# Performance work log

Hardware: AMD Instinct MI355X
Metric: run time of the kernel (lower is better)

The kernel has to match this reference:

```python
import jax, jax.numpy as jnp
import numpy as np

B, T, C, A, P = 16, 1024, 512, 4096, 256  # batch, frames, phones, allophone arcs, phonemes


def setup_inputs() -> dict:
    key = jax.random.key(0)
    k1, k2, k3 = jax.random.split(key, 3)
    hs_pad = jax.random.normal(k1, (B, T, C), dtype=jnp.float32)
    # each phone has exactly A // C allophone arcs (full coverage, balanced)
    phone_arc_labels = jnp.arange(A, dtype=jnp.int32) % C
    arcs_per_phone = A // C
    # weights near -log(arcs_per_phone) so sum_a exp(log_prob + w) ~= 1,
    # matching a trained allophone layer and keeping the redis step log-safe
    alloW = 0.01 * jax.random.normal(k2, (A,), dtype=jnp.float32) - jnp.log(
        jnp.float32(arcs_per_phone)
    )
    phoneme_arc_labels = jax.random.randint(k3, (A,), 0, P, dtype=jnp.int32)
    return {
        "hs_pad": hs_pad,
        "alloW": alloW,
        "phone_arc_labels": phone_arc_labels,
        "phoneme_arc_labels": phoneme_arc_labels,
        "n_phonemes": P,
    }


def reference(hs_pad, alloW, phone_arc_labels, phoneme_arc_labels, n_phonemes):
    # log_softmax over phones
    log_probs = jax.nn.log_softmax(hs_pad, axis=-1)  # [B,T,C]
    # WFST intersection of linear emission graph with 1-state allophone graph:
    # arc a gets weight log_probs[..., phone_label(a)] + alloW[a]
    new_emissions = log_probs[..., phone_arc_labels] + alloW  # [B,T,A]
    # squash many phones per phoneme: exp + scatter-add over output labels
    ex = jnp.exp(new_emissions)
    Bq, Tq = ex.shape[0], ex.shape[1]
    squashed = jnp.zeros((Bq, Tq, n_phonemes), dtype=ex.dtype)
    squashed = squashed.at[..., phoneme_arc_labels].add(ex)  # [B,T,P]
    # redistribute probability mass so it sums to 1
    redistributed = (squashed.sum(axis=-1) - 1.0)[..., None] / n_phonemes
    squashed = squashed - redistributed
    return jnp.log(squashed)
```

## Files before the change

kernel.cpp:

```cpp
#include <hip/hip_runtime.h>
#include <hip/hip_bf16.h>

#define BT   16384
#define CDIM 512
#define ADIM 4096
#define PDIM 256

typedef __attribute__((ext_vector_type(8))) short  short8;
typedef __attribute__((ext_vector_type(8))) unsigned short ushort8;
typedef __attribute__((ext_vector_type(4))) float  f32x4;

__device__ __forceinline__ unsigned short bf16_rne(float f) {
    unsigned int u = __float_as_uint(f);
    u += 0x7FFFu + ((u >> 16) & 1u);
    return (unsigned short)(u >> 16);
}

__global__ __launch_bounds__(256) void build_Wf(const float* __restrict__ alloW,
                                                const int* __restrict__ phone_lab,
                                                const int* __restrict__ phoneme_lab,
                                                unsigned short* __restrict__ Wf,
                                                float* __restrict__ rowsumW) {
    __shared__ float wrow[32 * PDIM];
    const int bx = blockIdx.x;
    const int t  = threadIdx.x;

#pragma unroll
    for (int i = 0; i < 32; ++i) wrow[i * 256 + t] = 0.0f;
    __syncthreads();

#pragma unroll
    for (int i = 0; i < ADIM / 256; ++i) {
        int a = i * 256 + t;
        int c = phone_lab[a];
        if ((c >> 5) == bx)
            atomicAdd(&wrow[(c & 31) * 256 + phoneme_lab[a]], __expf(alloW[a]));
    }
    __syncthreads();

    ushort8 pk[4];
#pragma unroll
    for (int g = 0; g < 4; ++g) {
#pragma unroll
        for (int j = 0; j < 8; ++j)
            pk[g][j] = bf16_rne(wrow[(g * 8 + j) * 256 + t]);
    }
    unsigned short* dst = Wf + (size_t)bx * (PDIM * 32) + t * 32;
#pragma unroll
    for (int g = 0; g < 4; ++g)
        *(ushort8*)(dst + g * 8) = pk[g];

    {
        const int i = t >> 3, j = t & 7;
        float s = 0.0f;
#pragma unroll
        for (int m = 0; m < 32; ++m) s += wrow[i * 256 + j * 32 + m];
        s += __shfl_xor(s, 1);
        s += __shfl_xor(s, 2);
        s += __shfl_xor(s, 4);
        if (j == 0) rowsumW[bx * 32 + i] = s;
    }
}

__global__ __launch_bounds__(256, 2) void allo_fused(const float* __restrict__ hs,
                                                     const unsigned short* __restrict__ Wf,
                                                     const float* __restrict__ rowsumW,
                                                     float* __restrict__ out) {
    __shared__ __align__(16) unsigned short Af[2 * 16 * 16 * 32];
    __shared__ float invZ[32];
    __shared__ float corrS[32];

    const int tid  = threadIdx.x;
    const int wave = tid >> 6;
    const int lane = tid & 63;
    const int row0 = blockIdx.x * 32;

    {
        const int r   = tid >> 3;
        const int ksl = tid & 7;
        const int rb  = r >> 4;
        const int cc  = r & 15;
        const float* hsr = hs + (size_t)(row0 + r) * CDIM + ksl * 4;
        const float* rsw = rowsumW + ksl * 4;
        unsigned short* af = Af + rb * 8192 + cc * 32 + ksl * 4;

        float s = 0.0f, sw = 0.0f;
#pragma unroll
        for (int h = 0; h < 2; ++h) {
            float4 v[8], w[8];
#pragma unroll
            for (int i = 0; i < 8; ++i) {
                v[i] = *(const float4*)(hsr + (h * 8 + i) * 32);
                w[i] = *(const float4*)(rsw + (h * 8 + i) * 32);
            }
#pragma unroll
            for (int i = 0; i < 8; ++i) {
                float e0 = __expf(v[i].x), e1 = __expf(v[i].y);
                float e2 = __expf(v[i].z), e3 = __expf(v[i].w);
                s += (e0 + e1) + (e2 + e3);
                sw = fmaf(e0, w[i].x, sw); sw = fmaf(e1, w[i].y, sw);
                sw = fmaf(e2, w[i].z, sw); sw = fmaf(e3, w[i].w, sw);
                ushort4 pk;
                pk.x = bf16_rne(e0); pk.y = bf16_rne(e1);
                pk.z = bf16_rne(e2); pk.w = bf16_rne(e3);
                *(ushort4*)(af + (h * 8 + i) * 512) = pk;
            }
        }
        s  += __shfl_xor(s, 1);  sw += __shfl_xor(sw, 1);
        s  += __shfl_xor(s, 2);  sw += __shfl_xor(sw, 2);
        s  += __shfl_xor(s, 4);  sw += __shfl_xor(sw, 4);
        if (ksl == 0) {
            const float iz = 1.0f / s;
            invZ[r]  = iz;
            corrS[r] = (sw * iz - 1.0f) * (1.0f / (float)PDIM);
        }
    }
    __syncthreads();

    const int c = lane & 15;
    const int q = lane >> 4;

    f32x4 acc[2][4];
#pragma unroll
    for (int rb = 0; rb < 2; ++rb)
#pragma unroll
        for (int cb = 0; cb < 4; ++cb)
            acc[rb][cb] = (f32x4){0.f, 0.f, 0.f, 0.f};

    const unsigned short* wb  = Wf + (size_t)(wave * 64 + c) * 32 + q * 8;
    const unsigned short* af0 = Af + c * 32 + q * 8;

#pragma unroll 4
    for (int kb = 0; kb < 16; ++kb) {
        short8 a0 = *(const short8*)(af0 + kb * 512);
        short8 a1 = *(const short8*)(af0 + 8192 + kb * 512);

        const unsigned short* wkb = wb + (size_t)kb * 8192;
        short8 b0 = *(const short8*)(wkb);
        short8 b1 = *(const short8*)(wkb + 512);
        short8 b2 = *(const short8*)(wkb + 1024);
        short8 b3 = *(const short8*)(wkb + 1536);

        acc[0][0] = __builtin_amdgcn_mfma_f32_16x16x32_bf16(a0, b0, acc[0][0], 0, 0, 0);
        acc[0][1] = __builtin_amdgcn_mfma_f32_16x16x32_bf16(a0, b1, acc[0][1], 0, 0, 0);
        acc[0][2] = __builtin_amdgcn_mfma_f32_16x16x32_bf16(a0, b2, acc[0][2], 0, 0, 0);
        acc[0][3] = __builtin_amdgcn_mfma_f32_16x16x32_bf16(a0, b3, acc[0][3], 0, 0, 0);
        acc[1][0] = __builtin_amdgcn_mfma_f32_16x16x32_bf16(a1, b0, acc[1][0], 0, 0, 0);
        acc[1][1] = __builtin_amdgcn_mfma_f32_16x16x32_bf16(a1, b1, acc[1][1], 0, 0, 0);
        acc[1][2] = __builtin_amdgcn_mfma_f32_16x16x32_bf16(a1, b2, acc[1][2], 0, 0, 0);
        acc[1][3] = __builtin_amdgcn_mfma_f32_16x16x32_bf16(a1, b3, acc[1][3], 0, 0, 0);
    }

#pragma unroll
    for (int rb = 0; rb < 2; ++rb)
#pragma unroll
        for (int r = 0; r < 4; ++r) {
            const int rr = rb * 16 + q * 4 + r;
            const float iz = invZ[rr];
            const float co = corrS[rr];
            float* orow = out + (size_t)(row0 + rr) * PDIM + wave * 64 + c;
#pragma unroll
            for (int cb = 0; cb < 4; ++cb)
                orow[cb * 16] = __logf(acc[rb][cb][r] * iz - co);
        }
}

extern "C" void kernel_launch(void* const* d_in, const int* in_sizes, int n_in,
                              void* d_out, int out_size, void* d_ws, size_t ws_size,
                              hipStream_t stream) {
    const float* hs          = (const float*)d_in[0];
    const float* alloW       = (const float*)d_in[1];
    const int*   phone_lab   = (const int*)d_in[2];
    const int*   phoneme_lab = (const int*)d_in[3];
    float*       out         = (float*)d_out;

    unsigned short* Wf      = (unsigned short*)d_ws;
    float*          rowsumW = (float*)((char*)d_ws + (256 << 10));

    build_Wf<<<CDIM / 32, 256, 0, stream>>>(alloW, phone_lab, phoneme_lab, Wf, rowsumW);
    allo_fused<<<BT / 32, 256, 0, stream>>>(hs, Wf, rowsumW, out);
}
```

Measured before the change: 99.70 us.

## Compute exp and bf16 A-fragments in registers inside MFMA loop, drop LDS staging

The A operand is no longer staged through shared memory. Each wave now loads hs directly in MFMA fragment layout, computes exp, the softmax sum and the weighted sum in registers, and packs bf16 fragments inline. The per-row normalizers are reduced with cross-lane shuffles instead of a shared-memory table, which removes the LDS round trip and the block barrier. In exchange, each of the 4 waves redundantly loads the same 32 hs rows and recomputes their exps, so exp work and L2 traffic for hs rise fourfold.

Result: slower. 112.3 us (+12.6%).

```diff
diff --git a/kernel.cpp b/kernel.cpp
--- a/kernel.cpp
+++ b/kernel.cpp
@@ -66,59 +66,17 @@
                                                      const unsigned short* __restrict__ Wf,
                                                      const float* __restrict__ rowsumW,
                                                      float* __restrict__ out) {
-    __shared__ __align__(16) unsigned short Af[2 * 16 * 16 * 32];
-    __shared__ float invZ[32];
-    __shared__ float corrS[32];
-
     const int tid  = threadIdx.x;
     const int wave = tid >> 6;
     const int lane = tid & 63;
+    const int c    = lane & 15;
+    const int q    = lane >> 4;
     const int row0 = blockIdx.x * 32;
 
-    {
-        const int r   = tid >> 3;
-        const int ksl = tid & 7;
-        const int rb  = r >> 4;
-        const int cc  = r & 15;
-        const float* hsr = hs + (size_t)(row0 + r) * CDIM + ksl * 4;
-        const float* rsw = rowsumW + ksl * 4;
-        unsigned short* af = Af + rb * 8192 + cc * 32 + ksl * 4;
-
-        float s = 0.0f, sw = 0.0f;
-#pragma unroll
-        for (int h = 0; h < 2; ++h) {
-            float4 v[8], w[8];
-#pragma unroll
-            for (int i = 0; i < 8; ++i) {
-                v[i] = *(const float4*)(hsr + (h * 8 + i) * 32);
-                w[i] = *(const float4*)(rsw + (h * 8 + i) * 32);
-            }
-#pragma unroll
-            for (int i = 0; i < 8; ++i) {
-                float e0 = __expf(v[i].x), e1 = __expf(v[i].y);
-                float e2 = __expf(v[i].z), e3 = __expf(v[i].w);
-                s += (e0 + e1) + (e2 + e3);
-                sw = fmaf(e0, w[i].x, sw); sw = fmaf(e1, w[i].y, sw);
-                sw = fmaf(e2, w[i].z, sw); sw = fmaf(e3, w[i].w, sw);
-                ushort4 pk;
-                pk.x = bf16_rne(e0); pk.y = bf16_rne(e1);
-                pk.z = bf16_rne(e2); pk.w = bf16_rne(e3);
-                *(ushort4*)(af + (h * 8 + i) * 512) = pk;
-            }
-        }
-        s  += __shfl_xor(s, 1);  sw += __shfl_xor(sw, 1);
-        s  += __shfl_xor(s, 2);  sw += __shfl_xor(sw, 2);
-        s  += __shfl_xor(s, 4);  sw += __shfl_xor(sw, 4);
-        if (ksl == 0) {
-            const float iz = 1.0f / s;
-            invZ[r]  = iz;
-            corrS[r] = (sw * iz - 1.0f) * (1.0f / (float)PDIM);
-        }
-    }
-    __syncthreads();
-
-    const int c = lane & 15;
-    const int q = lane >> 4;
+    const float* hsr0 = hs + (size_t)(row0 + c) * CDIM + q * 8;
+    const float* hsr1 = hsr0 + (size_t)16 * CDIM;
+    const float* rsw  = rowsumW + q * 8;
+    const unsigned short* wb = Wf + (size_t)(wave * 64 + c) * 32 + q * 8;
 
     f32x4 acc[2][4];
 #pragma unroll
@@ -127,19 +85,53 @@
         for (int cb = 0; cb < 4; ++cb)
             acc[rb][cb] = (f32x4){0.f, 0.f, 0.f, 0.f};
 
-    const unsigned short* wb  = Wf + (size_t)(wave * 64 + c) * 32 + q * 8;
-    const unsigned short* af0 = Af + c * 32 + q * 8;
+    float z0 = 0.f, z1 = 0.f, sw0 = 0.f, sw1 = 0.f;
 
 #pragma unroll 4
     for (int kb = 0; kb < 16; ++kb) {
-        short8 a0 = *(const short8*)(af0 + kb * 512);
-        short8 a1 = *(const short8*)(af0 + 8192 + kb * 512);
+        const int koff = kb * 32;
+        float4 v00 = *(const float4*)(hsr0 + koff);
+        float4 v01 = *(const float4*)(hsr0 + koff + 4);
+        float4 v10 = *(const float4*)(hsr1 + koff);
+        float4 v11 = *(const float4*)(hsr1 + koff + 4);
+        float4 w0  = *(const float4*)(rsw + koff);
+        float4 w1  = *(const float4*)(rsw + koff + 4);
 
         const unsigned short* wkb = wb + (size_t)kb * 8192;
         short8 b0 = *(const short8*)(wkb);
         short8 b1 = *(const short8*)(wkb + 512);
         short8 b2 = *(const short8*)(wkb + 1024);
         short8 b3 = *(const short8*)(wkb + 1536);
+
+        float e00 = __expf(v00.x), e01 = __expf(v00.y);
+        float e02 = __expf(v00.z), e03 = __expf(v00.w);
+        float e04 = __expf(v01.x), e05 = __expf(v01.y);
+        float e06 = __expf(v01.z), e07 = __expf(v01.w);
+        z0 += ((e00 + e01) + (e02 + e03)) + ((e04 + e05) + (e06 + e07));
+        sw0 = fmaf(e00, w0.x, sw0); sw0 = fmaf(e01, w0.y, sw0);
+        sw0 = fmaf(e02, w0.z, sw0); sw0 = fmaf(e03, w0.w, sw0);
+        sw0 = fmaf(e04, w1.x, sw0); sw0 = fmaf(e05, w1.y, sw0);
+        sw0 = fmaf(e06, w1.z, sw0); sw0 = fmaf(e07, w1.w, sw0);
+
+        float e10 = __expf(v10.x), e11 = __expf(v10.y);
+        float e12 = __expf(v10.z), e13 = __expf(v10.w);
+        float e14 = __expf(v11.x), e15 = __expf(v11.y);
+        float e16 = __expf(v11.z), e17 = __expf(v11.w);
+        z1 += ((e10 + e11) + (e12 + e13)) + ((e14 + e15) + (e16 + e17));
+        sw1 = fmaf(e10, w0.x, sw1); sw1 = fmaf(e11, w0.y, sw1);
+        sw1 = fmaf(e12, w0.z, sw1); sw1 = fmaf(e13, w0.w, sw1);
+        sw1 = fmaf(e14, w1.x, sw1); sw1 = fmaf(e15, w1.y, sw1);
+        sw1 = fmaf(e16, w1.z, sw1); sw1 = fmaf(e17, w1.w, sw1);
+
+        short8 a0, a1;
+        a0[0] = (short)bf16_rne(e00); a0[1] = (short)bf16_rne(e01);
+        a0[2] = (short)bf16_rne(e02); a0[3] = (short)bf16_rne(e03);
+        a0[4] = (short)bf16_rne(e04); a0[5] = (short)bf16_rne(e05);
+        a0[6] = (short)bf16_rne(e06); a0[7] = (short)bf16_rne(e07);
+        a1[0] = (short)bf16_rne(e10); a1[1] = (short)bf16_rne(e11);
+        a1[2] = (short)bf16_rne(e12); a1[3] = (short)bf16_rne(e13);
+        a1[4] = (short)bf16_rne(e14); a1[5] = (short)bf16_rne(e15);
+        a1[6] = (short)bf16_rne(e16); a1[7] = (short)bf16_rne(e17);
 
         acc[0][0] = __builtin_amdgcn_mfma_f32_16x16x32_bf16(a0, b0, acc[0][0], 0, 0, 0);
         acc[0][1] = __builtin_amdgcn_mfma_f32_16x16x32_bf16(a0, b1, acc[0][1], 0, 0, 0);
@@ -151,18 +143,35 @@
         acc[1][3] = __builtin_amdgcn_mfma_f32_16x16x32_bf16(a1, b3, acc[1][3], 0, 0, 0);
     }
 
+    z0  += __shfl_xor(z0, 16);  z0  += __shfl_xor(z0, 32);
+    z1  += __shfl_xor(z1, 16);  z1  += __shfl_xor(z1, 32);
+    sw0 += __shfl_xor(sw0, 16); sw0 += __shfl_xor(sw0, 32);
+    sw1 += __shfl_xor(sw1, 16); sw1 += __shfl_xor(sw1, 32);
+
+    const float iz0 = 1.0f / z0;
+    const float co0 = (sw0 * iz0 - 1.0f) * (1.0f / (float)PDIM);
+    const float iz1 = 1.0f / z1;
+    const float co1 = (sw1 * iz1 - 1.0f) * (1.0f / (float)PDIM);
+
+    float izA[4], coA[4], izB[4], coB[4];
 #pragma unroll
-    for (int rb = 0; rb < 2; ++rb)
+    for (int r = 0; r < 4; ++r) {
+        const int src = q * 4 + r;
+        izA[r] = __shfl(iz0, src); coA[r] = __shfl(co0, src);
+        izB[r] = __shfl(iz1, src); coB[r] = __shfl(co1, src);
+    }
+
 #pragma unroll
-        for (int r = 0; r < 4; ++r) {
-            const int rr = rb * 16 + q * 4 + r;
-            const float iz = invZ[rr];
-            const float co = corrS[rr];
-            float* orow = out + (size_t)(row0 + rr) * PDIM + wave * 64 + c;
+    for (int r = 0; r < 4; ++r) {
+        const int rr = q * 4 + r;
+        float* orow0 = out + (size_t)(row0 + rr) * PDIM + wave * 64 + c;
+        float* orow1 = out + (size_t)(row0 + 16 + rr) * PDIM + wave * 64 + c;
 #pragma unroll
-            for (int cb = 0; cb < 4; ++cb)
-                orow[cb * 16] = __logf(acc[rb][cb][r] * iz - co);
+        for (int cb = 0; cb < 4; ++cb) {
+            orow0[cb * 16] = __logf(acc[0][cb][r] * izA[r] - coA[r]);
+            orow1[cb * 16] = __logf(acc[1][cb][r] * izB[r] - coB[r]);
         }
+    }
 }
 
 extern "C" void kernel_launch(void* const* d_in, const int* in_sizes, int n_in,
```
